# Performance work log

Hardware: AMD Instinct MI355X
Metric: run time of the kernel (lower is better)

The kernel has to match this reference:

```python
import jax, jax.numpy as jnp
import numpy as np

B, V, NF, K = 16, 5000, 352, 120


def setup_inputs() -> dict:
    key = jax.random.key(0)
    k1, k2, k3, k4 = jax.random.split(key, 4)
    return {
        "feat_x": jax.random.normal(k1, (B, V, NF), dtype=jnp.float32),
        "feat_y": jax.random.normal(k2, (B, V, NF), dtype=jnp.float32),
        "evecs_x": jax.random.normal(k3, (B, V, K), dtype=jnp.float32),
        "evecs_y": jax.random.normal(k4, (B, V, K), dtype=jnp.float32),
    }


def reference(feat_x, feat_y, evecs_x, evecs_y):
    # Spectral coefficients: F_hat[b] = (evecs_x[b]^T feat_x[b])^T -> [B, F, K]
    F_hat = jnp.einsum("bvk,bvf->bfk", evecs_x, feat_x)
    G_hat = jnp.einsum("bvk,bvf->bfk", evecs_y, feat_y)

    # C1[b] = (inv(F^T F) F^T G)^T, batched least-squares solve
    FtF = jnp.einsum("bfk,bfl->bkl", F_hat, F_hat)  # [B,K,K]
    FtG = jnp.einsum("bfk,bfl->bkl", F_hat, G_hat)  # [B,K,K]
    C1 = jnp.linalg.solve(FtF, FtG).transpose(0, 2, 1)

    GtG = jnp.einsum("bfk,bfl->bkl", G_hat, G_hat)
    GtF = jnp.einsum("bfk,bfl->bkl", G_hat, F_hat)
    C2 = jnp.linalg.solve(GtG, GtF).transpose(0, 2, 1)
    return (C1, C2)
```

## Files before the change

kernel.cpp:

```cpp
#include <hip/hip_runtime.h>
#include <hip/hip_bf16.h>

#define NB 16
#define VV 5000
#define NFD 352
#define KD 120
#define NCH 5
#define SLABSZ (352 * 120)

typedef __attribute__((ext_vector_type(8))) short short8;
typedef __attribute__((ext_vector_type(4))) float float4v;

__device__ __forceinline__ unsigned short bfb(float a) {
    return __builtin_bit_cast(unsigned short, __float2bfloat16(a));
}

__device__ __forceinline__ void pack8(const float* f, int4& hi, int4& lo) {
    unsigned short h[8], l[8];
    #pragma unroll
    for (int j = 0; j < 8; ++j) {
        const float a = f[j];
        const __hip_bfloat16 hb = __float2bfloat16(a);
        h[j] = __builtin_bit_cast(unsigned short, hb);
        l[j] = bfb(a - __bfloat162float(hb));
    }
    hi.x = h[0] | (h[1] << 16); hi.y = h[2] | (h[3] << 16);
    hi.z = h[4] | (h[5] << 16); hi.w = h[6] | (h[7] << 16);
    lo.x = l[0] | (l[1] << 16); lo.y = l[2] | (l[3] << 16);
    lo.z = l[4] | (l[5] << 16); lo.w = l[6] | (l[7] << 16);
}

__global__ __launch_bounds__(256, 2) void proj_mfma(
    const float* __restrict__ fx, const float* __restrict__ fy,
    const float* __restrict__ ex, const float* __restrict__ ey,
    float* __restrict__ partials)
{
    const int t  = threadIdx.x;
    const int mt = blockIdx.x % 3;
    const int ch = blockIdx.x / 3;
    const int wh = blockIdx.y;
    const int b  = blockIdx.z;

    const float* Ab = (wh ? fy : fx) + (size_t)b * VV * NFD;
    const float* Bb = (wh ? ey : ex) + (size_t)b * VV * KD;
    const int m0 = mt * 128;

    __shared__ int4 smem4[4096];
    unsigned char* smem = (unsigned char*)smem4;

    int aoff[4], awb[4], ao[4];
    #pragma unroll
    for (int i = 0; i < 4; ++i) {
        const int q = i * 256 + t;
        const int m = q & 127;
        const int o = q >> 7;
        const int col = min(m0 + m, NFD - 1);
        aoff[i] = col + o * 8 * NFD;
        awb[i]  = m * 128 + ((o ^ (m & 7)) * 16);
        ao[i]   = o;
    }
    int boff[4], bwb[4], bo[4];
    #pragma unroll
    for (int i = 0; i < 4; ++i) {
        const int q = i * 256 + t;
        const int n = q & 127;
        const int o = q >> 7;
        const int col = min(n, KD - 1);
        boff[i] = col + o * 8 * KD;
        bwb[i]  = 32768 + n * 128 + ((o ^ (n & 7)) * 16);
        bo[i]   = o;
    }

    const int lane = t & 63;
    const int wid  = t >> 6;
    const int wm = wid >> 1, wn = wid & 1;
    const int r16 = lane & 15;
    const int g   = lane >> 4;

    int abase[4], bbase[4];
    #pragma unroll
    for (int mf = 0; mf < 4; ++mf) {
        const int m = wm * 64 + mf * 16 + r16;
        abase[mf] = m * 128 + ((g ^ (m & 7)) * 16);
    }
    #pragma unroll
    for (int nf = 0; nf < 4; ++nf) {
        const int n = wn * 64 + nf * 16 + r16;
        bbase[nf] = 32768 + n * 128 + ((g ^ (n & 7)) * 16);
    }

    float4v acc[4][4];
    #pragma unroll
    for (int mf = 0; mf < 4; ++mf)
        #pragma unroll
        for (int nf = 0; nf < 4; ++nf)
            acc[mf][nf] = float4v{0.f, 0.f, 0.f, 0.f};

    const int step0 = ch * 16;
    const int nst   = (ch < 4) ? 16 : 15;

    float fa[4][8], fb[4][8];

    auto do_loads = [&](int v0) {
        const int va = v0 * NFD;
        const int vb = v0 * KD;
        if (v0 + 64 <= VV) {
            #pragma unroll
            for (int i = 0; i < 4; ++i)
                #pragma unroll
                for (int j = 0; j < 8; ++j)
                    fa[i][j] = Ab[aoff[i] + va + j * NFD];
            #pragma unroll
            for (int i = 0; i < 4; ++i)
                #pragma unroll
                for (int j = 0; j < 8; ++j)
                    fb[i][j] = Bb[boff[i] + vb + j * KD];
        } else {
            #pragma unroll
            for (int i = 0; i < 4; ++i)
                #pragma unroll
                for (int j = 0; j < 8; ++j) {
                    const int v = v0 + ao[i] * 8 + j;
                    fa[i][j] = (v < VV) ? Ab[aoff[i] + va + j * NFD] : 0.f;
                }
            #pragma unroll
            for (int i = 0; i < 4; ++i)
                #pragma unroll
                for (int j = 0; j < 8; ++j) {
                    const int v = v0 + bo[i] * 8 + j;
                    fb[i][j] = (v < VV) ? Bb[boff[i] + vb + j * KD] : 0.f;
                }
        }
    };
    auto do_writes = [&]() {
        #pragma unroll
        for (int i = 0; i < 4; ++i) {
            int4 hi, lo;
            pack8(fa[i], hi, lo);
            *(int4*)(smem + awb[i])         = hi;
            *(int4*)(smem + awb[i] + 16384) = lo;
        }
        #pragma unroll
        for (int i = 0; i < 4; ++i) {
            int4 hi, lo;
            pack8(fb[i], hi, lo);
            *(int4*)(smem + bwb[i])         = hi;
            *(int4*)(smem + bwb[i] + 16384) = lo;
        }
    };

    do_loads(step0 * 64);
    do_writes();
    __syncthreads();

    for (int st = 0; st < nst; ++st) {
        const bool more = (st + 1 < nst);
        if (more) do_loads((step0 + st + 1) * 64);

        #pragma unroll
        for (int ks = 0; ks < 2; ++ks) {
            short8 ah[4], al[4], bh[4], bl[4];
            #pragma unroll
            for (int mf = 0; mf < 4; ++mf) {
                const int ad = abase[mf] ^ (ks * 64);
                ah[mf] = *(const short8*)(smem + ad);
                al[mf] = *(const short8*)(smem + ad + 16384);
            }
            #pragma unroll
            for (int nf = 0; nf < 4; ++nf) {
                const int bd = bbase[nf] ^ (ks * 64);
                bh[nf] = *(const short8*)(smem + bd);
                bl[nf] = *(const short8*)(smem + bd + 16384);
            }
            #pragma unroll
            for (int mf = 0; mf < 4; ++mf)
                #pragma unroll
                for (int nf = 0; nf < 4; ++nf) {
                    acc[mf][nf] = __builtin_amdgcn_mfma_f32_16x16x32_bf16(ah[mf], bh[nf], acc[mf][nf], 0, 0, 0);
                    acc[mf][nf] = __builtin_amdgcn_mfma_f32_16x16x32_bf16(ah[mf], bl[nf], acc[mf][nf], 0, 0, 0);
                    acc[mf][nf] = __builtin_amdgcn_mfma_f32_16x16x32_bf16(al[mf], bh[nf], acc[mf][nf], 0, 0, 0);
                }
        }
        __syncthreads();
        if (more) {
            do_writes();
            __syncthreads();
        }
    }

    float* slab = partials + (size_t)((ch * 2 + wh) * NB + b) * SLABSZ;
    #pragma unroll
    for (int mf = 0; mf < 4; ++mf) {
        const int mrow = mt * 128 + wm * 64 + mf * 16 + g * 4;
        #pragma unroll
        for (int nf = 0; nf < 4; ++nf) {
            const int n = wn * 64 + nf * 16 + r16;
            if (n < KD) {
                #pragma unroll
                for (int r = 0; r < 4; ++r) {
                    const int m = mrow + r;
                    if (m < NFD) slab[(size_t)m * KD + n] = acc[mf][nf][r];
                }
            }
        }
    }
}

__global__ __launch_bounds__(256) void reduce_k(
    const float* __restrict__ partials, float* __restrict__ fhat, float* __restrict__ ghat)
{
    const int id = blockIdx.x * 256 + threadIdx.x;
    if (id >= NFD * KD) return;
    const int wb = blockIdx.y;
    const int wh = wb >> 4;
    const int b  = wb & 15;

    const float* p = partials + (size_t)(wh * NB + b) * SLABSZ + id;
    const size_t chstride = (size_t)2 * NB * SLABSZ;

    float s = 0.f;
    #pragma unroll
    for (int c = 0; c < NCH; ++c) s += p[c * chstride];

    float* dst = (wh ? ghat : fhat) + (size_t)b * NFD * KD + id;
    *dst = s;
}

__device__ __forceinline__ void gemm_tn_64x64(
    const float* __restrict__ A, const float* __restrict__ B, float* __restrict__ C,
    int V, int M, int N, int m0, int n0)
{
    __shared__ float As[16][64];
    __shared__ float Bs[16][64];

    const int tid = threadIdx.x;
    const int tx = tid & 15;
    const int ty = tid >> 4;
    const int sr = tid >> 4;
    const int sc = (tid & 15) << 2;

    float acc[4][4] = {{0.f,0.f,0.f,0.f},{0.f,0.f,0.f,0.f},
                       {0.f,0.f,0.f,0.f},{0.f,0.f,0.f,0.f}};

    for (int v0 = 0; v0 < V; v0 += 16) {
        const int v = v0 + sr;
        float4 av; av.x = av.y = av.z = av.w = 0.f;
        float4 bv; bv.x = bv.y = bv.z = bv.w = 0.f;
        if (v < V) {
            const float* Ar = A + (size_t)v * M;
            const int ca = m0 + sc;
            if (ca + 3 < M) {
                av = *(const float4*)(Ar + ca);
            } else {
                if (ca + 0 < M) av.x = Ar[ca + 0];
                if (ca + 1 < M) av.y = Ar[ca + 1];
                if (ca + 2 < M) av.z = Ar[ca + 2];
                if (ca + 3 < M) av.w = Ar[ca + 3];
            }
            const float* Br = B + (size_t)v * N;
            const int cb = n0 + sc;
            if (cb + 3 < N) {
                bv = *(const float4*)(Br + cb);
            } else {
                if (cb + 0 < N) bv.x = Br[cb + 0];
                if (cb + 1 < N) bv.y = Br[cb + 1];
                if (cb + 2 < N) bv.z = Br[cb + 2];
                if (cb + 3 < N) bv.w = Br[cb + 3];
            }
        }
        __syncthreads();
        *(float4*)&As[sr][sc] = av;
        *(float4*)&Bs[sr][sc] = bv;
        __syncthreads();

        #pragma unroll
        for (int kk = 0; kk < 16; ++kk) {
            const float4 a4 = *(const float4*)&As[kk][ty << 2];
            const float4 b4 = *(const float4*)&Bs[kk][tx << 2];
            const float a[4]  = {a4.x, a4.y, a4.z, a4.w};
            const float bb[4] = {b4.x, b4.y, b4.z, b4.w};
            #pragma unroll
            for (int i = 0; i < 4; ++i)
                #pragma unroll
                for (int j = 0; j < 4; ++j)
                    acc[i][j] = fmaf(a[i], bb[j], acc[i][j]);
        }
    }

    #pragma unroll
    for (int i = 0; i < 4; ++i) {
        const int m = m0 + (ty << 2) + i;
        if (m < M) {
            #pragma unroll
            for (int j = 0; j < 4; ++j) {
                const int n = n0 + (tx << 2) + j;
                if (n < N) C[(size_t)m * N + n] = acc[i][j];
            }
        }
    }
}

__global__ __launch_bounds__(256) void gram_kernel(
    const float* __restrict__ fhat, const float* __restrict__ ghat,
    float* __restrict__ ftf, float* __restrict__ gtg, float* __restrict__ ftg)
{
    const int b = blockIdx.z;
    const int which = blockIdx.y;
    const int m0 = (blockIdx.x & 1) * 64;
    const int n0 = (blockIdx.x >> 1) * 64;

    const float* F = fhat + (size_t)b * NFD * KD;
    const float* G = ghat + (size_t)b * NFD * KD;
    const float* A  = (which == 1) ? G : F;
    const float* Bp = (which == 0) ? F : G;
    float* C = ((which == 0) ? ftf : (which == 1) ? gtg : ftg) + (size_t)b * KD * KD;

    gemm_tn_64x64(A, Bp, C, NFD, KD, KD, m0, n0);
}

__device__ __forceinline__ float ldval(const float* __restrict__ A, const float* __restrict__ B,
                                       int pair, int row, int col) {
    if (col < KD) return A[row * KD + col];
    const int l = col - KD;
    return pair ? B[l * KD + row] : B[row * KD + l];
}

#define FOR15(OP) OP(0) OP(1) OP(2) OP(3) OP(4) OP(5) OP(6) OP(7) OP(8) OP(9) \
                  OP(10) OP(11) OP(12) OP(13) OP(14)

__global__ __launch_bounds__(480, 1) void solve_kernel(
    const float* __restrict__ ftf, const float* __restrict__ gtg,
    const float* __restrict__ ftg, float* __restrict__ out)
{
    const int pair = blockIdx.x;
    const int b = blockIdx.y;
    const int tid = threadIdx.x;
    const int cg = tid & 15;
    const int rg = tid >> 4;
    const int cbase = cg * 15;
    const int r0 = rg * 4;
    const int seg = cg * 20;

    const float* Ag = ((pair == 0) ? ftf : gtg) + (size_t)b * KD * KD;
    const float* Bg = ftg + (size_t)b * KD * KD;

    __shared__ __align__(16) float prow[2][320];
    __shared__ __align__(16) float pcol[2][120];

    #define DECL(I) float w##I = ldval(Ag, Bg, pair, r0 + 0, cbase + (I)); \
                    float x##I = ldval(Ag, Bg, pair, r0 + 1, cbase + (I)); \
                    float y##I = ldval(Ag, Bg, pair, r0 + 2, cbase + (I)); \
                    float z##I = ldval(Ag, Bg, pair, r0 + 3, cbase + (I));
    FOR15(DECL)
    #undef DECL

    if (rg == 0) {
        #define PUB0(I) prow[0][seg + (I)] = w##I;
        FOR15(PUB0)
        #undef PUB0
    }
    if (cg == 0) *(float4*)&pcol[0][r0] = float4{w0, x0, y0, z0};
    __syncthreads();

    int jseg = 0, joff = 0;

    for (int j = 0; j < KD; ++j) {
        const int cur = j & 1;
        const int nxt = cur ^ 1;

        const float pinv = 1.0f / prow[cur][jseg * 20 + joff];
        const float4 f4 = *(const float4*)&pcol[cur][r0];

        const float4 q0 = *(const float4*)&prow[cur][seg + 0];
        const float4 q1 = *(const float4*)&prow[cur][seg + 4];
        const float4 q2 = *(const float4*)&prow[cur][seg + 8];
        const float4 q3 = *(const float4*)&prow[cur][seg + 12];
        const float p0 = q0.x, p1 = q0.y, p2 = q0.z, p3 = q0.w;
        const float p4 = q1.x, p5 = q1.y, p6 = q1.z, p7 = q1.w;
        const float p8 = q2.x, p9 = q2.y, p10 = q2.z, p11 = q2.w;
        const float p12 = q3.x, p13 = q3.y, p14 = q3.z;

        const float fw = f4.x * pinv, fx = f4.y * pinv;
        const float fy = f4.z * pinv, fz = f4.w * pinv;

        #define UPD(I) w##I = fmaf(-fw, p##I, w##I); x##I = fmaf(-fx, p##I, x##I); \
                       y##I = fmaf(-fy, p##I, y##I); z##I = fmaf(-fz, p##I, z##I);
        FOR15(UPD)
        #undef UPD

        if (rg == (j >> 2)) {
            #define FW(I) w##I = p##I * pinv;
            #define FX(I) x##I = p##I * pinv;
            #define FY(I) y##I = p##I * pinv;
            #define FZ(I) z##I = p##I * pinv;
            switch (j & 3) {
                case 0: FOR15(FW) break;
                case 1: FOR15(FX) break;
                case 2: FOR15(FY) break;
                default: FOR15(FZ) break;
            }
            #undef FW
            #undef FX
            #undef FY
            #undef FZ
        }

        const int j2 = j + 1;

        if (j2 < KD && rg == (j2 >> 2)) {
            #define PW(I) prow[nxt][seg + (I)] = w##I;
            #define PX(I) prow[nxt][seg + (I)] = x##I;
            #define PY(I) prow[nxt][seg + (I)] = y##I;
            #define PZ(I) prow[nxt][seg + (I)] = z##I;
            switch (j2 & 3) {
                case 0: FOR15(PW) break;
                case 1: FOR15(PX) break;
                case 2: FOR15(PY) break;
                default: FOR15(PZ) break;
            }
            #undef PW
            #undef PX
            #undef PY
            #undef PZ
        }

        joff++; if (joff == 15) { joff = 0; jseg++; }
        if (j2 < KD && cg == jseg) {
            #define PC(I) case I: *(float4*)&pcol[nxt][r0] = float4{w##I, x##I, y##I, z##I}; break;
            switch (joff) {
                FOR15(PC)
                default: break;
            }
            #undef PC
        }
        __syncthreads();
    }

    if (cg >= 8) {
        float* op = out + (size_t)pair * NB * KD * KD + (size_t)b * KD * KD;
        #define OUTW(I) { const int l = cbase + (I) - KD; \
                          *(float4*)&op[l * KD + r0] = float4{w##I, x##I, y##I, z##I}; }
        FOR15(OUTW)
        #undef OUTW
    }
}

extern "C" void kernel_launch(void* const* d_in, const int* in_sizes, int n_in,
                              void* d_out, int out_size, void* d_ws, size_t ws_size,
                              hipStream_t stream)
{
    const float* feat_x  = (const float*)d_in[0];
    const float* feat_y  = (const float*)d_in[1];
    const float* evecs_x = (const float*)d_in[2];
    const float* evecs_y = (const float*)d_in[3];
    float* out = (float*)d_out;

    float* ws       = (float*)d_ws;
    float* partials = ws;
    float* fhat     = partials + (size_t)NCH * 2 * NB * SLABSZ;
    float* ghat     = fhat + (size_t)NB * NFD * KD;
    float* ftf      = ws;
    float* gtg      = ftf + (size_t)NB * KD * KD;
    float* ftg      = gtg + (size_t)NB * KD * KD;

    proj_mfma <<<dim3(15, 2, NB), 256, 0, stream>>>(feat_x, feat_y, evecs_x, evecs_y, partials);
    reduce_k  <<<dim3(165, 32), 256, 0, stream>>>(partials, fhat, ghat);
    gram_kernel<<<dim3(4, 3, NB), 256, 0, stream>>>(fhat, ghat, ftf, gtg, ftg);
    solve_kernel<<<dim3(2, NB), 480, 0, stream>>>(ftf, gtg, ftg, out);
}
```

Before: 211.0 us.

## Double-buffer LDS with 32-row K steps and remap block order

```diff
diff --git a/kernel.cpp b/kernel.cpp
--- a/kernel.cpp
+++ b/kernel.cpp
@@ -35,11 +35,16 @@
     const float* __restrict__ ex, const float* __restrict__ ey,
     float* __restrict__ partials)
 {
-    const int t  = threadIdx.x;
-    const int mt = blockIdx.x % 3;
-    const int ch = blockIdx.x / 3;
-    const int wh = blockIdx.y;
-    const int b  = blockIdx.z;
+    const int t = threadIdx.x;
+
+    int lin = blockIdx.x + 15 * (blockIdx.y + 2 * blockIdx.z);
+    lin = (lin & 7) * 60 + (lin >> 3);
+    const int xx   = lin % 15;
+    const int rest = lin / 15;
+    const int wh = rest & 1;
+    const int b  = rest >> 1;
+    const int mt = xx % 3;
+    const int ch = xx / 3;
 
     const float* Ab = (wh ? fy : fx) + (size_t)b * VV * NFD;
     const float* Bb = (wh ? ey : ex) + (size_t)b * VV * KD;
@@ -48,26 +53,24 @@
     __shared__ int4 smem4[4096];
     unsigned char* smem = (unsigned char*)smem4;
 
-    int aoff[4], awb[4], ao[4];
-    #pragma unroll
-    for (int i = 0; i < 4; ++i) {
+    int acol[2], awb[2], ao[2];
+    #pragma unroll
+    for (int i = 0; i < 2; ++i) {
         const int q = i * 256 + t;
         const int m = q & 127;
         const int o = q >> 7;
-        const int col = min(m0 + m, NFD - 1);
-        aoff[i] = col + o * 8 * NFD;
-        awb[i]  = m * 128 + ((o ^ (m & 7)) * 16);
+        acol[i] = min(m0 + m, NFD - 1);
+        awb[i]  = m * 64 + ((o ^ ((m >> 1) & 3)) * 16);
         ao[i]   = o;
     }
-    int boff[4], bwb[4], bo[4];
-    #pragma unroll
-    for (int i = 0; i < 4; ++i) {
+    int bcol[2], bwb[2], bo[2];
+    #pragma unroll
+    for (int i = 0; i < 2; ++i) {
         const int q = i * 256 + t;
         const int n = q & 127;
         const int o = q >> 7;
-        const int col = min(n, KD - 1);
-        boff[i] = col + o * 8 * KD;
-        bwb[i]  = 32768 + n * 128 + ((o ^ (n & 7)) * 16);
+        bcol[i] = min(n, KD - 1);
+        bwb[i]  = n * 64 + ((o ^ ((n >> 1) & 3)) * 16);
         bo[i]   = o;
     }
 
@@ -81,12 +84,12 @@
     #pragma unroll
     for (int mf = 0; mf < 4; ++mf) {
         const int m = wm * 64 + mf * 16 + r16;
-        abase[mf] = m * 128 + ((g ^ (m & 7)) * 16);
+        abase[mf] = m * 64 + ((g ^ ((m >> 1) & 3)) * 16);
     }
     #pragma unroll
     for (int nf = 0; nf < 4; ++nf) {
         const int n = wn * 64 + nf * 16 + r16;
-        bbase[nf] = 32768 + n * 128 + ((g ^ (n & 7)) * 16);
+        bbase[nf] = n * 64 + ((g ^ ((n >> 1) & 3)) * 16);
     }
 
     float4v acc[4][4];
@@ -96,96 +99,102 @@
         for (int nf = 0; nf < 4; ++nf)
             acc[mf][nf] = float4v{0.f, 0.f, 0.f, 0.f};
 
-    const int step0 = ch * 16;
-    const int nst   = (ch < 4) ? 16 : 15;
-
-    float fa[4][8], fb[4][8];
-
-    auto do_loads = [&](int v0) {
-        const int va = v0 * NFD;
-        const int vb = v0 * KD;
-        if (v0 + 64 <= VV) {
-            #pragma unroll
-            for (int i = 0; i < 4; ++i)
-                #pragma unroll
-                for (int j = 0; j < 8; ++j)
-                    fa[i][j] = Ab[aoff[i] + va + j * NFD];
-            #pragma unroll
-            for (int i = 0; i < 4; ++i)
-                #pragma unroll
-                for (int j = 0; j < 8; ++j)
-                    fb[i][j] = Bb[boff[i] + vb + j * KD];
+    const int step0 = ch * 32;
+    const int nst   = (ch < 4) ? 32 : 30;
+
+    float faP[2][8], fbP[2][8], faQ[2][8], fbQ[2][8];
+
+    auto do_loads = [&](int st, float (&fa)[2][8], float (&fb)[2][8]) {
+        const int v0 = (step0 + st) * 32;
+        if (v0 + 32 <= VV) {
+            #pragma unroll
+            for (int i = 0; i < 2; ++i) {
+                const float* pa = Ab + (size_t)(v0 + ao[i] * 8) * NFD + acol[i];
+                #pragma unroll
+                for (int j = 0; j < 8; ++j) fa[i][j] = pa[j * NFD];
+            }
+            #pragma unroll
+            for (int i = 0; i < 2; ++i) {
+                const float* pb = Bb + (size_t)(v0 + bo[i] * 8) * KD + bcol[i];
+                #pragma unroll
+                for (int j = 0; j < 8; ++j) fb[i][j] = pb[j * KD];
+            }
         } else {
             #pragma unroll
-            for (int i = 0; i < 4; ++i)
+            for (int i = 0; i < 2; ++i) {
+                const float* pa = Ab + (size_t)(v0 + ao[i] * 8) * NFD + acol[i];
                 #pragma unroll
                 for (int j = 0; j < 8; ++j) {
                     const int v = v0 + ao[i] * 8 + j;
-                    fa[i][j] = (v < VV) ? Ab[aoff[i] + va + j * NFD] : 0.f;
+                    fa[i][j] = (v < VV) ? pa[j * NFD] : 0.f;
                 }
-            #pragma unroll
-            for (int i = 0; i < 4; ++i)
+            }
+            #pragma unroll
+            for (int i = 0; i < 2; ++i) {
+                const float* pb = Bb + (size_t)(v0 + bo[i] * 8) * KD + bcol[i];
                 #pragma unroll
                 for (int j = 0; j < 8; ++j) {
                     const int v = v0 + bo[i] * 8 + j;
-                    fb[i][j] = (v < VV) ? Bb[boff[i] + vb + j * KD] : 0.f;
+                    fb[i][j] = (v < VV) ? pb[j * KD] : 0.f;
                 }
+            }
         }
     };
-    auto do_writes = [&]() {
-        #pragma unroll
-        for (int i = 0; i < 4; ++i) {
+
+    auto do_writes = [&](int bufb, float (&fa)[2][8], float (&fb)[2][8]) {
+        #pragma unroll
+        for (int i = 0; i < 2; ++i) {
             int4 hi, lo;
             pack8(fa[i], hi, lo);
-            *(int4*)(smem + awb[i])         = hi;
-            *(int4*)(smem + awb[i] + 16384) = lo;
-        }
-        #pragma unroll
-        for (int i = 0; i < 4; ++i) {
+            *(int4*)(smem + bufb + awb[i])        = hi;
+            *(int4*)(smem + bufb + awb[i] + 8192) = lo;
+        }
+        #pragma unroll
+        for (int i = 0; i < 2; ++i) {
             int4 hi, lo;
             pack8(fb[i], hi, lo);
-            *(int4*)(smem + bwb[i])         = hi;
-            *(int4*)(smem + bwb[i] + 16384) = lo;
+            *(int4*)(smem + bufb + 16384 + bwb[i]) = hi;
+            *(int4*)(smem + bufb + 24576 + bwb[i]) = lo;
         }
     };
 
-    do_loads(step0 * 64);
-    do_writes();
+    auto compute = [&](int bufb) {
+        short8 ah[4], al[4], bh[4], bl[4];
+        #pragma unroll
+        for (int mf = 0; mf < 4; ++mf) {
+            ah[mf] = *(const short8*)(smem + bufb + abase[mf]);
+            al[mf] = *(const short8*)(smem + bufb + abase[mf] + 8192);
+        }
+        #pragma unroll
+        for (int nf = 0; nf < 4; ++nf) {
+            bh[nf] = *(const short8*)(smem + bufb + 16384 + bbase[nf]);
+            bl[nf] = *(const short8*)(smem + bufb + 24576 + bbase[nf]);
+        }
+        #pragma unroll
+        for (int mf = 0; mf < 4; ++mf)
+            #pragma unroll
+            for (int nf = 0; nf < 4; ++nf) {
+                acc[mf][nf] = __builtin_amdgcn_mfma_f32_16x16x32_bf16(ah[mf], bh[nf], acc[mf][nf], 0, 0, 0);
+                acc[mf][nf] = __builtin_amdgcn_mfma_f32_16x16x32_bf16(ah[mf], bl[nf], acc[mf][nf], 0, 0, 0);
+                acc[mf][nf] = __builtin_amdgcn_mfma_f32_16x16x32_bf16(al[mf], bh[nf], acc[mf][nf], 0, 0, 0);
+            }
+    };
+
+    do_loads(0, faP, fbP);
+    do_loads(1, faQ, fbQ);
+    do_writes(0, faP, fbP);
     __syncthreads();
 
-    for (int st = 0; st < nst; ++st) {
-        const bool more = (st + 1 < nst);
-        if (more) do_loads((step0 + st + 1) * 64);
-
-        #pragma unroll
-        for (int ks = 0; ks < 2; ++ks) {
-            short8 ah[4], al[4], bh[4], bl[4];
-            #pragma unroll
-            for (int mf = 0; mf < 4; ++mf) {
-                const int ad = abase[mf] ^ (ks * 64);
-                ah[mf] = *(const short8*)(smem + ad);
-                al[mf] = *(const short8*)(smem + ad + 16384);
-            }
-            #pragma unroll
-            for (int nf = 0; nf < 4; ++nf) {
-                const int bd = bbase[nf] ^ (ks * 64);
-                bh[nf] = *(const short8*)(smem + bd);
-                bl[nf] = *(const short8*)(smem + bd + 16384);
-            }
-            #pragma unroll
-            for (int mf = 0; mf < 4; ++mf)
-                #pragma unroll
-                for (int nf = 0; nf < 4; ++nf) {
-                    acc[mf][nf] = __builtin_amdgcn_mfma_f32_16x16x32_bf16(ah[mf], bh[nf], acc[mf][nf], 0, 0, 0);
-                    acc[mf][nf] = __builtin_amdgcn_mfma_f32_16x16x32_bf16(ah[mf], bl[nf], acc[mf][nf], 0, 0, 0);
-                    acc[mf][nf] = __builtin_amdgcn_mfma_f32_16x16x32_bf16(al[mf], bh[nf], acc[mf][nf], 0, 0, 0);
-                }
-        }
+    for (int i = 0; i < nst / 2; ++i) {
+        const int st = 2 * i;
+        if (st + 2 < nst) do_loads(st + 2, faP, fbP);
+        compute(0);
+        do_writes(32768, faQ, fbQ);
         __syncthreads();
-        if (more) {
-            do_writes();
-            __syncthreads();
-        }
+        if (st + 3 < nst) do_loads(st + 3, faQ, fbQ);
+        compute(32768);
+        if (st + 2 < nst) do_writes(0, faP, fbP);
+        __syncthreads();
     }
 
     float* slab = partials + (size_t)((ch * 2 + wh) * NB + b) * SLABSZ;
```

New measurement: 208.8 us (median of 2 runs). Within noise of the previous version (-1.0%).
